# Kernel tuning notes

Hardware: AMD Instinct MI355X
Metric: run time of the kernel (lower is better)

The kernel has to match this reference:

```python
import jax, jax.numpy as jnp
import numpy as np

N, H, HEADS = 4096, 256, 3
ALPHA = 0.2
NEG_INF = -9e15


def _sign_adj(key, n, density):
    # sparse signed adjacency with +1 on the diagonal (values in {-1,0,1})
    k1, k2 = jax.random.split(key)
    mask = jax.random.uniform(k1, (n, n)) < density
    sign = jnp.where(jax.random.uniform(k2, (n, n)) < 0.5, -1.0, 1.0)
    adj = jnp.where(mask, sign, 0.0).astype(jnp.float32)
    idx = jnp.arange(n)
    return adj.at[idx, idx].set(1.0)


def setup_inputs() -> dict:
    key = jax.random.key(0)
    ks = jax.random.split(key, 16)
    std = 0.01
    gain = 1.414
    return {
        "h": jax.random.normal(ks[0], (N, H), jnp.float32),
        "node_adj": _sign_adj(ks[1], N, 0.005),
        "edge_adj": _sign_adj(ks[2], N, 0.005),
        "gat_W": jax.random.normal(ks[3], (HEADS, H, H), jnp.float32) * (gain / np.sqrt(H, dtype=np.float32)),
        "gat_a": jax.random.normal(ks[4], (HEADS, 2 * H, 1), jnp.float32) * 0.1,
        "edge_Wih": jax.random.normal(ks[5], (3 * H, H), jnp.float32) * std,
        "edge_Whh": jax.random.normal(ks[6], (3 * H, H), jnp.float32) * std,
        "edge_bih": jnp.zeros((3 * H,), jnp.float32),
        "edge_bhh": jnp.zeros((3 * H,), jnp.float32),
        "node_Wih": jax.random.normal(ks[7], (3 * H, H), jnp.float32) * std,
        "node_Whh": jax.random.normal(ks[8], (3 * H, H), jnp.float32) * std,
        "node_bih": jnp.zeros((3 * H,), jnp.float32),
        "node_bhh": jnp.zeros((3 * H,), jnp.float32),
    }


def _gru_cell(x, hstate, Wih, Whh, bih, bhh):
    # torch.nn.GRUCell math, gate order [r, z, n]
    gi = x @ Wih.T + bih
    gh = hstate @ Whh.T + bhh
    ir, iz, inn = jnp.split(gi, 3, axis=1)
    hr, hz, hn = jnp.split(gh, 3, axis=1)
    r = jax.nn.sigmoid(ir + hr)
    z = jax.nn.sigmoid(iz + hz)
    n = jnp.tanh(inn + r * hn)
    return (1.0 - z) * n + z * hstate


def _gat_head(h, node_adj, edge_adj, W, a):
    hW = h @ W  # [N,H]
    hp = (node_adj > 0).astype(hW.dtype) @ hW
    hm = (node_adj < 0).astype(hW.dtype) @ hW
    e_plus = jax.nn.leaky_relu(jnp.concatenate([hp, hm], axis=1) @ a, ALPHA)[:, 0]   # [N]
    e_minus = jax.nn.leaky_relu(jnp.concatenate([hm, hp], axis=1) @ a, ALPHA)[:, 0]  # [N]
    # attention[i, j] depends only on column j (original builds this via repeat)
    att = jnp.where(edge_adj > 0, e_plus[None, :], NEG_INF)
    att = jnp.where(edge_adj < 0, e_minus[None, :], att)
    att = jax.nn.softmax(att, axis=1)
    return (att * edge_adj) @ hW  # concat=False -> no elu


def reference(h, node_adj, edge_adj, gat_W, gat_a,
              edge_Wih, edge_Whh, edge_bih, edge_bhh,
              node_Wih, node_Whh, node_bih, node_bhh):
    dn = jnp.diag(node_adj)  # [N]
    de = jnp.diag(edge_adj)  # [N]
    idx = jnp.arange(node_adj.shape[0])
    node_adj_norm = node_adj.at[idx, idx].add(-dn)  # zero diagonal
    edge_adj_norm = edge_adj.at[idx, idx].add(-de)

    # msg_type == 'diff'
    node_support = node_adj_norm @ h
    edge_output = _gru_cell(node_support, h, edge_Wih, edge_Whh, edge_bih, edge_bhh)

    edge_support = _gat_head(h, node_adj_norm, edge_adj_norm, gat_W[0], gat_a[0])
    for i in range(1, HEADS):
        edge_support = edge_support + _gat_head(h, node_adj_norm, edge_adj_norm, gat_W[i], gat_a[i])
    edge_support = edge_support / HEADS

    node_output = _gru_cell(edge_support, h, node_Wih, node_Whh, node_bih, node_bhh)

    # sp.mm(I_edge, edge_output) + sp.mm(I_node, node_output)
    return de[:, None] * edge_output + dn[:, None] * node_output
```

## Files before the change

### kernel.cpp

```cpp
#include <hip/hip_runtime.h>
#include <hip/hip_bf16.h>
#include <math.h>

#define NN 4096
#define HH 256
#define G3 768
#define NHEADS 3
#define MAXE 128
#define ALPHA 0.2f

typedef __bf16 bf16;
typedef __attribute__((ext_vector_type(2))) __bf16 bf16x2;
typedef __attribute__((ext_vector_type(4))) __bf16 bf16x4;
typedef __attribute__((ext_vector_type(8))) __bf16 bf16x8;
typedef __attribute__((ext_vector_type(4))) float f32x4;

__device__ __forceinline__ void async_copy16(void* lds, const void* g) {
    __builtin_amdgcn_global_load_lds((const __attribute__((address_space(1))) void*)g,
                                     (__attribute__((address_space(3))) void*)lds, 16, 0, 0);
}

__device__ inline float lrelu(float x) { return x > 0.f ? x : ALPHA * x; }
__device__ inline float sigm(float x) { return 1.f / (1.f + __expf(-x)); }

__global__ __launch_bounds__(256) void prep_k(
    const float* __restrict__ h,
    const float* __restrict__ eWih, const float* __restrict__ eWhh,
    const float* __restrict__ nWih, const float* __restrict__ nWhh,
    const float* __restrict__ gat_W, const float* __restrict__ gat_a,
    bf16* __restrict__ hb,
    bf16* __restrict__ Weib, bf16* __restrict__ Wehb,
    bf16* __restrict__ Wnib, bf16* __restrict__ Wnhb,
    bf16* __restrict__ Wtb, float* __restrict__ c0, float* __restrict__ c1) {
    __shared__ float tile[32][33];
    __shared__ float a_s[512];
    int b = blockIdx.x, t = threadIdx.x;
    if (b < 1024) {
        int idx = b * 256 + t;
        float4 v = *(const float4*)(h + (size_t)idx * 4);
        bf16x4 o = {(bf16)v.x, (bf16)v.y, (bf16)v.z, (bf16)v.w};
        *(bf16x4*)(hb + (size_t)idx * 4) = o;
    } else if (b < 1792) {
        int w = (b - 1024) / 192;
        int idx = ((b - 1024) % 192) * 256 + t;
        const float* in = w == 0 ? eWih : (w == 1 ? eWhh : (w == 2 ? nWih : nWhh));
        bf16* outp = w == 0 ? Weib : (w == 1 ? Wehb : (w == 2 ? Wnib : Wnhb));
        float4 v = *(const float4*)(in + (size_t)idx * 4);
        bf16x4 o = {(bf16)v.x, (bf16)v.y, (bf16)v.z, (bf16)v.w};
        *(bf16x4*)(outp + (size_t)idx * 4) = o;
    } else if (b < 1984) {
        int b2 = b - 1792;
        int hd = b2 >> 6, tl = b2 & 63;
        int k0 = (tl >> 3) * 32, n0 = (tl & 7) * 32;
        int tx = t % 32, ty = t / 32;
        const float* Wh = gat_W + (size_t)hd * HH * HH;
        for (int r = ty; r < 32; r += 8) tile[r][tx] = Wh[(size_t)(k0 + r) * HH + n0 + tx];
        __syncthreads();
        bf16* Wth = Wtb + (size_t)hd * HH * HH;
        for (int r = ty; r < 32; r += 8) Wth[(size_t)(n0 + r) * HH + k0 + tx] = (bf16)tile[tx][r];
    } else {
        int hd = b - 1984;
        a_s[t] = gat_a[(size_t)hd * 512 + t];
        a_s[t + 256] = gat_a[(size_t)hd * 512 + 256 + t];
        __syncthreads();
        const float* Wr = gat_W + (size_t)hd * HH * HH + (size_t)t * HH;
        f32x4 s0v = {}, s1v = {};
#pragma unroll 8
        for (int c4 = 0; c4 < 64; c4++) {
            f32x4 w = *(const f32x4*)(Wr + c4 * 4);
            f32x4 a0 = *(const f32x4*)(a_s + c4 * 4);
            f32x4 a1 = *(const f32x4*)(a_s + 256 + c4 * 4);
            s0v += w * a0;
            s1v += w * a1;
        }
        c0[hd * HH + t] = s0v[0] + s0v[1] + s0v[2] + s0v[3];
        c1[hd * HH + t] = s1v[0] + s1v[1] + s1v[2] + s1v[3];
    }
}

__global__ __launch_bounds__(256) void compact_k(
    const float* __restrict__ node_adj, const float* __restrict__ edge_adj,
    float* __restrict__ dn, float* __restrict__ de,
    int* __restrict__ ccols_n, int* __restrict__ nnz_n,
    int* __restrict__ ccols_e, int* __restrict__ nnz_e) {
    int b = blockIdx.x, t = threadIdx.x;
    bool node = b < NN;
    int i = node ? b : b - NN;
    __shared__ int cnt;
    __shared__ int cols_s[MAXE];
    if (t == 0) cnt = 0;
    __syncthreads();
    const float* rp = (node ? node_adj : edge_adj) + (size_t)i * NN + t * 16;

    f32x4 v0 = *(const f32x4*)(rp);
    f32x4 v1 = *(const f32x4*)(rp + 4);
    f32x4 v2 = *(const f32x4*)(rp + 8);
    f32x4 v3 = *(const f32x4*)(rp + 12);
    int j0 = t * 16;

    int k = 0;
#define CNT(A, J) { float a_ = (A); if (a_ != 0.f) { if ((J) == i) (node ? dn : de)[i] = a_; else k++; } }
    CNT(v0[0], j0)      CNT(v0[1], j0 + 1)  CNT(v0[2], j0 + 2)  CNT(v0[3], j0 + 3)
    CNT(v1[0], j0 + 4)  CNT(v1[1], j0 + 5)  CNT(v1[2], j0 + 6)  CNT(v1[3], j0 + 7)
    CNT(v2[0], j0 + 8)  CNT(v2[1], j0 + 9)  CNT(v2[2], j0 + 10) CNT(v2[3], j0 + 11)
    CNT(v3[0], j0 + 12) CNT(v3[1], j0 + 13) CNT(v3[2], j0 + 14) CNT(v3[3], j0 + 15)
#undef CNT

    int base = 0;
    if (k) base = atomicAdd(&cnt, k);

#define WRT(A, J) { float a_ = (A); if (a_ != 0.f && (J) != i) { \
        if (base < MAXE) cols_s[base] = (a_ > 0.f) ? ((J) + 1) : -((J) + 1); base++; } }
    WRT(v0[0], j0)      WRT(v0[1], j0 + 1)  WRT(v0[2], j0 + 2)  WRT(v0[3], j0 + 3)
    WRT(v1[0], j0 + 4)  WRT(v1[1], j0 + 5)  WRT(v1[2], j0 + 6)  WRT(v1[3], j0 + 7)
    WRT(v2[0], j0 + 8)  WRT(v2[1], j0 + 9)  WRT(v2[2], j0 + 10) WRT(v2[3], j0 + 11)
    WRT(v3[0], j0 + 12) WRT(v3[1], j0 + 13) WRT(v3[2], j0 + 14) WRT(v3[3], j0 + 15)
#undef WRT

    __syncthreads();
    int n = cnt < MAXE ? cnt : MAXE;
    int* cg = (node ? ccols_n : ccols_e) + (size_t)i * MAXE;
    if (t == 0) (node ? nnz_n : nnz_e)[i] = n;
    if (t < n) cg[t] = cols_s[t];
}

__global__ __launch_bounds__(256) void gather_k(
    const int* __restrict__ ccols_n, const int* __restrict__ nnz_n,
    const bf16* __restrict__ hb,
    const float* __restrict__ c0, const float* __restrict__ c1,
    bf16* __restrict__ nsupb, float* __restrict__ ep, float* __restrict__ em) {
    int i = blockIdx.x, t = threadIdx.x, lane = t & 63, wid = t >> 6;
    __shared__ int cols_s[MAXE];
    __shared__ float part[6][4];
    int n = nnz_n[i];
    if (n > MAXE) n = MAXE;
    if (t < n) cols_s[t] = ccols_n[(size_t)i * MAXE + t];
    __syncthreads();
    float accp = 0.f, accm = 0.f;
#pragma unroll 8
    for (int kk = 0; kk < n; kk++) {
        int c = cols_s[kk];
        int j = (c > 0 ? c : -c) - 1;
        float hv = (float)hb[(size_t)j * HH + t];
        if (c > 0) accp += hv; else accm += hv;
    }
    nsupb[(size_t)i * HH + t] = (bf16)(accp - accm);
    float u[6];
#pragma unroll
    for (int hd = 0; hd < NHEADS; hd++) {
        float a0 = c0[hd * HH + t], a1 = c1[hd * HH + t];
        u[hd * 2]     = accp * a0 + accm * a1;
        u[hd * 2 + 1] = accm * a0 + accp * a1;
    }
#pragma unroll
    for (int vv = 0; vv < 6; vv++)
#pragma unroll
        for (int off = 32; off; off >>= 1) u[vv] += __shfl_xor(u[vv], off);
    if (lane == 0)
#pragma unroll
        for (int vv = 0; vv < 6; vv++) part[vv][wid] = u[vv];
    __syncthreads();
    if (t < 6) {
        float s = part[t][0] + part[t][1] + part[t][2] + part[t][3];
        int hd = t >> 1;
        ((t & 1) == 0 ? ep : em)[(size_t)hd * NN + i] = lrelu(s);
    }
}

__global__ __launch_bounds__(256) void gemm_bt(
    const bf16* __restrict__ A0, const bf16* __restrict__ A1, const bf16* __restrict__ A2,
    const bf16* __restrict__ B0, const bf16* __restrict__ B1, const bf16* __restrict__ B2,
    bf16* __restrict__ C0, bf16* __restrict__ C1, bf16* __restrict__ C2) {
    __shared__ bf16 a_s[128 * 32];
    __shared__ bf16 b_s[128 * 32];
    int z = blockIdx.z;
    const bf16* A = z == 0 ? A0 : (z == 1 ? A1 : A2);
    const bf16* Bt = z == 0 ? B0 : (z == 1 ? B1 : B2);
    bf16* C = z == 0 ? C0 : (z == 1 ? C1 : C2);

    int tid = threadIdx.x;
    int lane = tid & 63, wid = tid >> 6;
    int wr = (wid >> 1) * 64, wc = (wid & 1) * 64;
    int i0 = blockIdx.x * 128;
    int c0n = blockIdx.y * 128;

    f32x4 acc[4][4] = {};
    int kq = (lane >> 4) * 8;

    for (int k0 = 0; k0 < 256; k0 += 32) {
        __syncthreads();
#pragma unroll
        for (int it = 0; it < 2; it++) {
            int ch = it * 256 + tid;
            int r = ch >> 2, c16 = ch & 3;
            async_copy16(&a_s[ch * 8], A + (size_t)(i0 + r) * 256 + k0 + c16 * 8);
            async_copy16(&b_s[ch * 8], Bt + (size_t)(c0n + r) * 256 + k0 + c16 * 8);
        }
        __syncthreads();
        bf16x8 af[4], bf[4];
#pragma unroll
        for (int m = 0; m < 4; m++) af[m] = *(const bf16x8*)&a_s[(wr + m * 16 + (lane & 15)) * 32 + kq];
#pragma unroll
        for (int n = 0; n < 4; n++) bf[n] = *(const bf16x8*)&b_s[(wc + n * 16 + (lane & 15)) * 32 + kq];
#pragma unroll
        for (int m = 0; m < 4; m++)
#pragma unroll
            for (int n = 0; n < 4; n++)
                acc[m][n] = __builtin_amdgcn_mfma_f32_16x16x32_bf16(af[m], bf[n], acc[m][n], 0, 0, 0);
    }
#pragma unroll
    for (int m = 0; m < 4; m++) {
#pragma unroll
        for (int n = 0; n < 4; n++) {
            int row = i0 + wr + m * 16 + (lane >> 4) * 4;
            int col = c0n + wc + n * 16 + (lane & 15);
#pragma unroll
            for (int j = 0; j < 4; j++)
                C[(size_t)(row + j) * G3 + col] = (bf16)acc[m][n][j];
        }
    }
}

__global__ __launch_bounds__(256) void gat_out(
    const int* __restrict__ ccols_e, const int* __restrict__ nnz_e,
    const float* __restrict__ ep, const float* __restrict__ em,
    const bf16* __restrict__ hWb2, bf16* __restrict__ esupb) {
    int i = blockIdx.x, t = threadIdx.x;
    __shared__ int cols_s[MAXE];
    __shared__ int js[MAXE];
    __shared__ float w_s[NHEADS][MAXE];
    __shared__ f32x4 sacc[NHEADS][64];
    int n = nnz_e[i];
    if (n > MAXE) n = MAXE;
    if (t < n) {
        int c = ccols_e[(size_t)i * MAXE + t];
        cols_s[t] = c;
        js[t] = (c > 0 ? c : -c) - 1;
    }
    __syncthreads();
    int wid = t >> 6, lane = t & 63;
    if (wid < NHEADS) {
        int hd = wid;
        const float* eph = ep + (size_t)hd * NN;
        const float* emh = em + (size_t)hd * NN;
        float v0 = -1e30f, v1 = -1e30f;
        if (lane < n)      { int c = cols_s[lane];      v0 = c > 0 ? eph[js[lane]]      : emh[js[lane]]; }
        if (lane + 64 < n) { int c = cols_s[lane + 64]; v1 = c > 0 ? eph[js[lane + 64]] : emh[js[lane + 64]]; }
        float mx = fmaxf(v0, v1);
#pragma unroll
        for (int off = 32; off; off >>= 1) mx = fmaxf(mx, __shfl_xor(mx, off));
        float w0 = (lane < n) ? __expf(v0 - mx) : 0.f;
        float w1 = (lane + 64 < n) ? __expf(v1 - mx) : 0.f;
        float s = w0 + w1;
#pragma unroll
        for (int off = 32; off; off >>= 1) s += __shfl_xor(s, off);
        float inv = 1.f / s;
        if (lane < n)      w_s[hd][lane]      = (cols_s[lane] > 0 ? w0 : -w0) * inv;
        if (lane + 64 < n) w_s[hd][lane + 64] = (cols_s[lane + 64] > 0 ? w1 : -w1) * inv;
    }
    __syncthreads();
    if (t < 192) {
        int hd = t >> 6, g = t & 63;
        const bf16* base = hWb2 + (size_t)hd * HH + g * 4;
        f32x4 acc = {};
#pragma unroll 4
        for (int k = 0; k < n; k++) {
            float w = w_s[hd][k];
            bf16x4 hv = *(const bf16x4*)(base + (size_t)js[k] * G3);
            f32x4 f = {(float)hv[0], (float)hv[1], (float)hv[2], (float)hv[3]};
            acc += w * f;
        }
        sacc[hd][g] = acc;
    }
    __syncthreads();
    if (t < 64) {
        f32x4 s = (sacc[0][t] + sacc[1][t] + sacc[2][t]) * (1.f / 3.f);
        bf16x4 o = {(bf16)s[0], (bf16)s[1], (bf16)s[2], (bf16)s[3]};
        *(bf16x4*)(esupb + (size_t)i * HH + t * 4) = o;
    }
}

__global__ __launch_bounds__(256) void gru_both(
    const bf16* __restrict__ gie, const bf16* __restrict__ ghe,
    const bf16* __restrict__ gin, const bf16* __restrict__ ghn,
    const float* __restrict__ ebih, const float* __restrict__ ebhh,
    const float* __restrict__ nbih, const float* __restrict__ nbhh,
    const float* __restrict__ h, const float* __restrict__ dnv, const float* __restrict__ dev,
    float* __restrict__ out) {
    int sub = threadIdx.x >> 7, tc = threadIdx.x & 127;
    int i = blockIdx.x * 2 + sub;
    int c = tc * 2;
    size_t gb = (size_t)i * G3;
    float2 hv = *(const float2*)(h + (size_t)i * HH + c);
    float De = dev[i], Dn = dnv[i];

#define LD2(p, off) (*(const bf16x2*)((p) + gb + (off) + c))
#define BI2(p, off) (*(const float2*)((p) + (off) + c))
    bf16x2 eir = LD2(gie, 0), eiz = LD2(gie, 256), ein = LD2(gie, 512);
    bf16x2 ehr = LD2(ghe, 0), ehz = LD2(ghe, 256), ehn = LD2(ghe, 512);
    bf16x2 nir = LD2(gin, 0), niz = LD2(gin, 256), nin = LD2(gin, 512);
    bf16x2 nhr = LD2(ghn, 0), nhz = LD2(ghn, 256), nhn = LD2(ghn, 512);
    float2 ebr = BI2(ebih, 0), ebz = BI2(ebih, 256), ebn = BI2(ebih, 512);
    float2 eb2r = BI2(ebhh, 0), eb2z = BI2(ebhh, 256), eb2n = BI2(ebhh, 512);
    float2 nbr = BI2(nbih, 0), nbz = BI2(nbih, 256), nbn = BI2(nbih, 512);
    float2 nb2r = BI2(nbhh, 0), nb2z = BI2(nbhh, 256), nb2n = BI2(nbhh, 512);
#undef LD2
#undef BI2

    float res[2];
#pragma unroll
    for (int j = 0; j < 2; j++) {
        float hj = j == 0 ? hv.x : hv.y;
        float r = sigm(((float)eir[j] + (j ? ebr.y : ebr.x)) + ((float)ehr[j] + (j ? eb2r.y : eb2r.x)));
        float z = sigm(((float)eiz[j] + (j ? ebz.y : ebz.x)) + ((float)ehz[j] + (j ? eb2z.y : eb2z.x)));
        float nv = tanhf(((float)ein[j] + (j ? ebn.y : ebn.x)) + r * ((float)ehn[j] + (j ? eb2n.y : eb2n.x)));
        float eo = (1.f - z) * nv + z * hj;
        float r2 = sigm(((float)nir[j] + (j ? nbr.y : nbr.x)) + ((float)nhr[j] + (j ? nb2r.y : nb2r.x)));
        float z2 = sigm(((float)niz[j] + (j ? nbz.y : nbz.x)) + ((float)nhz[j] + (j ? nb2z.y : nb2z.x)));
        float nv2 = tanhf(((float)nin[j] + (j ? nbn.y : nbn.x)) + r2 * ((float)nhn[j] + (j ? nb2n.y : nb2n.x)));
        float no = (1.f - z2) * nv2 + z2 * hj;
        res[j] = De * eo + Dn * no;
    }
    *(float2*)(out + (size_t)i * HH + c) = make_float2(res[0], res[1]);
}

extern "C" void kernel_launch(void* const* d_in, const int* in_sizes, int n_in,
                              void* d_out, int out_size, void* d_ws, size_t ws_size,
                              hipStream_t stream) {
    const float* h        = (const float*)d_in[0];
    const float* node_adj = (const float*)d_in[1];
    const float* edge_adj = (const float*)d_in[2];
    const float* gat_W    = (const float*)d_in[3];
    const float* gat_a    = (const float*)d_in[4];
    const float* e_Wih    = (const float*)d_in[5];
    const float* e_Whh    = (const float*)d_in[6];
    const float* e_bih    = (const float*)d_in[7];
    const float* e_bhh    = (const float*)d_in[8];
    const float* n_Wih    = (const float*)d_in[9];
    const float* n_Whh    = (const float*)d_in[10];
    const float* n_bih    = (const float*)d_in[11];
    const float* n_bhh    = (const float*)d_in[12];
    float* out = (float*)d_out;

    char* ws = (char*)d_ws;
    size_t off = 0;
    auto alloc = [&](size_t bytes) { char* p = ws + off; off += (bytes + 255) & ~(size_t)255; return p; };

    float* ep    = (float*)alloc((size_t)NHEADS * NN * 4);
    float* em    = (float*)alloc((size_t)NHEADS * NN * 4);
    float* c0    = (float*)alloc((size_t)NHEADS * HH * 4);
    float* c1    = (float*)alloc((size_t)NHEADS * HH * 4);
    float* dn    = (float*)alloc(NN * 4);
    float* de    = (float*)alloc(NN * 4);
    bf16*  hb    = (bf16*)alloc((size_t)NN * HH * 2);
    bf16*  nsupb = (bf16*)alloc((size_t)NN * HH * 2);
    bf16*  esupb = (bf16*)alloc((size_t)NN * HH * 2);
    bf16*  hWb2  = (bf16*)alloc((size_t)NN * G3 * 2);
    bf16*  gie   = (bf16*)alloc((size_t)NN * G3 * 2);
    bf16*  ghe   = (bf16*)alloc((size_t)NN * G3 * 2);
    bf16*  gin   = (bf16*)alloc((size_t)NN * G3 * 2);
    bf16*  ghn   = (bf16*)alloc((size_t)NN * G3 * 2);
    bf16*  Weib  = (bf16*)alloc((size_t)G3 * HH * 2);
    bf16*  Wehb  = (bf16*)alloc((size_t)G3 * HH * 2);
    bf16*  Wnib  = (bf16*)alloc((size_t)G3 * HH * 2);
    bf16*  Wnhb  = (bf16*)alloc((size_t)G3 * HH * 2);
    bf16*  Wtb   = (bf16*)alloc((size_t)NHEADS * HH * HH * 2);
    int*   ccols_n = (int*)alloc((size_t)NN * MAXE * 4);
    int*   nnz_n   = (int*)alloc(NN * 4);
    int*   ccols_e = (int*)alloc((size_t)NN * MAXE * 4);
    int*   nnz_e   = (int*)alloc(NN * 4);

    dim3 b256(256);

    compact_k<<<2 * NN, b256, 0, stream>>>(node_adj, edge_adj, dn, de,
                                           ccols_n, nnz_n, ccols_e, nnz_e);

    prep_k<<<1987, b256, 0, stream>>>(h, e_Wih, e_Whh, n_Wih, n_Whh, gat_W, gat_a,
                                      hb, Weib, Wehb, Wnib, Wnhb, Wtb, c0, c1);

    gather_k<<<NN, b256, 0, stream>>>(ccols_n, nnz_n, hb, c0, c1, nsupb, ep, em);

    gemm_bt<<<dim3(NN / 128, G3 / 128, 3), b256, 0, stream>>>(
        hb, nsupb, hb, Wtb, Weib, Wehb, hWb2, gie, ghe);

    gat_out<<<NN, b256, 0, stream>>>(ccols_e, nnz_e, ep, em, hWb2, esupb);

    gemm_bt<<<dim3(NN / 128, G3 / 128, 2), b256, 0, stream>>>(
        esupb, hb, hb, Wnib, Wnhb, Wnhb, gin, ghn, ghn);

    gru_both<<<NN / 2, b256, 0, stream>>>(gie, ghe, gin, ghn,
                                          e_bih, e_bhh, n_bih, n_bhh,
                                          h, dn, de, out);
}
```

Before: 95.43 us.

## Fuse adjacency compaction with h-dependent GEMMs into one heterogeneous kernel

Merges the adjacency compaction kernel with the three GEMMs that depend only on h (hW for the GAT heads, and the hidden-state projections for both GRUs) into one launch. Blocks are split by index into GEMM tiles and compaction rows. The remaining GEMM launch now handles only the two input-dependent projections (node support and edge support). This removes launches and lets the memory-bound compaction overlap with MFMA work, but the compaction rows are permuted and the GEMM tiles use a simpler non-pipelined loop.

```diff
diff --git a/kernel.cpp b/kernel.cpp
--- a/kernel.cpp
+++ b/kernel.cpp
@@ -78,50 +78,102 @@
     }
 }
 
-__global__ __launch_bounds__(256) void compact_k(
+#define NGEMM 576
+__global__ __launch_bounds__(256) void mega_k(
     const float* __restrict__ node_adj, const float* __restrict__ edge_adj,
     float* __restrict__ dn, float* __restrict__ de,
     int* __restrict__ ccols_n, int* __restrict__ nnz_n,
-    int* __restrict__ ccols_e, int* __restrict__ nnz_e) {
-    int b = blockIdx.x, t = threadIdx.x;
-    bool node = b < NN;
-    int i = node ? b : b - NN;
+    int* __restrict__ ccols_e, int* __restrict__ nnz_e,
+    const bf16* __restrict__ hb, const bf16* __restrict__ Wtb,
+    const bf16* __restrict__ Wehb, const bf16* __restrict__ Wnhb,
+    bf16* __restrict__ hWb2, bf16* __restrict__ ghe, bf16* __restrict__ ghn) {
+    __shared__ bf16 a_s[128 * 32];
+    __shared__ bf16 b_s[128 * 32];
     __shared__ int cnt;
     __shared__ int cols_s[MAXE];
-    if (t == 0) cnt = 0;
-    __syncthreads();
-    const float* rp = (node ? node_adj : edge_adj) + (size_t)i * NN + t * 16;
-
-    f32x4 v0 = *(const f32x4*)(rp);
-    f32x4 v1 = *(const f32x4*)(rp + 4);
-    f32x4 v2 = *(const f32x4*)(rp + 8);
-    f32x4 v3 = *(const f32x4*)(rp + 12);
-    int j0 = t * 16;
-
-    int k = 0;
+    int bid = blockIdx.x, t = threadIdx.x;
+
+    if (bid < NGEMM) {
+        int z = bid / 192, r = bid % 192;
+        int i0 = (r % 32) * 128;
+        int c0n = (r / 32) * 128;
+        const bf16* Bt = z == 0 ? Wtb : (z == 1 ? Wehb : Wnhb);
+        bf16* C = z == 0 ? hWb2 : (z == 1 ? ghe : ghn);
+
+        int lane = t & 63, wid = t >> 6;
+        int wr = (wid >> 1) * 64, wc = (wid & 1) * 64;
+        f32x4 acc[4][4] = {};
+        int kq = (lane >> 4) * 8;
+
+        for (int k0 = 0; k0 < 256; k0 += 32) {
+            __syncthreads();
+#pragma unroll
+            for (int it = 0; it < 2; it++) {
+                int ch = it * 256 + t;
+                int rr = ch >> 2, c16 = ch & 3;
+                async_copy16(&a_s[ch * 8], hb + (size_t)(i0 + rr) * 256 + k0 + c16 * 8);
+                async_copy16(&b_s[ch * 8], Bt + (size_t)(c0n + rr) * 256 + k0 + c16 * 8);
+            }
+            __syncthreads();
+            bf16x8 af[4], bf[4];
+#pragma unroll
+            for (int m = 0; m < 4; m++) af[m] = *(const bf16x8*)&a_s[(wr + m * 16 + (lane & 15)) * 32 + kq];
+#pragma unroll
+            for (int n = 0; n < 4; n++) bf[n] = *(const bf16x8*)&b_s[(wc + n * 16 + (lane & 15)) * 32 + kq];
+#pragma unroll
+            for (int m = 0; m < 4; m++)
+#pragma unroll
+                for (int n = 0; n < 4; n++)
+                    acc[m][n] = __builtin_amdgcn_mfma_f32_16x16x32_bf16(af[m], bf[n], acc[m][n], 0, 0, 0);
+        }
+#pragma unroll
+        for (int m = 0; m < 4; m++) {
+#pragma unroll
+            for (int n = 0; n < 4; n++) {
+                int row = i0 + wr + m * 16 + (lane >> 4) * 4;
+                int col = c0n + wc + n * 16 + (lane & 15);
+#pragma unroll
+                for (int j = 0; j < 4; j++)
+                    C[(size_t)(row + j) * G3 + col] = (bf16)acc[m][n][j];
+            }
+        }
+    } else {
+        int g2 = bid - NGEMM;
+        int gs = (g2 & 7) * 1024 + (g2 >> 3);
+        bool node = gs < NN;
+        int i = node ? gs : gs - NN;
+        if (t == 0) cnt = 0;
+        __syncthreads();
+        const float* rp = (node ? node_adj : edge_adj) + (size_t)i * NN + t * 16;
+
+        f32x4 v0 = *(const f32x4*)(rp);
+        f32x4 v1 = *(const f32x4*)(rp + 4);
+        f32x4 v2 = *(const f32x4*)(rp + 8);
+        f32x4 v3 = *(const f32x4*)(rp + 12);
+        int j0 = t * 16;
+
+        int k = 0;
 #define CNT(A, J) { float a_ = (A); if (a_ != 0.f) { if ((J) == i) (node ? dn : de)[i] = a_; else k++; } }
-    CNT(v0[0], j0)      CNT(v0[1], j0 + 1)  CNT(v0[2], j0 + 2)  CNT(v0[3], j0 + 3)
-    CNT(v1[0], j0 + 4)  CNT(v1[1], j0 + 5)  CNT(v1[2], j0 + 6)  CNT(v1[3], j0 + 7)
-    CNT(v2[0], j0 + 8)  CNT(v2[1], j0 + 9)  CNT(v2[2], j0 + 10) CNT(v2[3], j0 + 11)
-    CNT(v3[0], j0 + 12) CNT(v3[1], j0 + 13) CNT(v3[2], j0 + 14) CNT(v3[3], j0 + 15)
+        CNT(v0[0], j0)      CNT(v0[1], j0 + 1)  CNT(v0[2], j0 + 2)  CNT(v0[3], j0 + 3)
+        CNT(v1[0], j0 + 4)  CNT(v1[1], j0 + 5)  CNT(v1[2], j0 + 6)  CNT(v1[3], j0 + 7)
+        CNT(v2[0], j0 + 8)  CNT(v2[1], j0 + 9)  CNT(v2[2], j0 + 10) CNT(v2[3], j0 + 11)
+        CNT(v3[0], j0 + 12) CNT(v3[1], j0 + 13) CNT(v3[2], j0 + 14) CNT(v3[3], j0 + 15)
 #undef CNT
-
-    int base = 0;
-    if (k) base = atomicAdd(&cnt, k);
-
+        int base = 0;
+        if (k) base = atomicAdd(&cnt, k);
 #define WRT(A, J) { float a_ = (A); if (a_ != 0.f && (J) != i) { \
-        if (base < MAXE) cols_s[base] = (a_ > 0.f) ? ((J) + 1) : -((J) + 1); base++; } }
-    WRT(v0[0], j0)      WRT(v0[1], j0 + 1)  WRT(v0[2], j0 + 2)  WRT(v0[3], j0 + 3)
-    WRT(v1[0], j0 + 4)  WRT(v1[1], j0 + 5)  WRT(v1[2], j0 + 6)  WRT(v1[3], j0 + 7)
-    WRT(v2[0], j0 + 8)  WRT(v2[1], j0 + 9)  WRT(v2[2], j0 + 10) WRT(v2[3], j0 + 11)
-    WRT(v3[0], j0 + 12) WRT(v3[1], j0 + 13) WRT(v3[2], j0 + 14) WRT(v3[3], j0 + 15)
+            if (base < MAXE) cols_s[base] = (a_ > 0.f) ? ((J) + 1) : -((J) + 1); base++; } }
+        WRT(v0[0], j0)      WRT(v0[1], j0 + 1)  WRT(v0[2], j0 + 2)  WRT(v0[3], j0 + 3)
+        WRT(v1[0], j0 + 4)  WRT(v1[1], j0 + 5)  WRT(v1[2], j0 + 6)  WRT(v1[3], j0 + 7)
+        WRT(v2[0], j0 + 8)  WRT(v2[1], j0 + 9)  WRT(v2[2], j0 + 10) WRT(v2[3], j0 + 11)
+        WRT(v3[0], j0 + 12) WRT(v3[1], j0 + 13) WRT(v3[2], j0 + 14) WRT(v3[3], j0 + 15)
 #undef WRT
-
-    __syncthreads();
-    int n = cnt < MAXE ? cnt : MAXE;
-    int* cg = (node ? ccols_n : ccols_e) + (size_t)i * MAXE;
-    if (t == 0) (node ? nnz_n : nnz_e)[i] = n;
-    if (t < n) cg[t] = cols_s[t];
+        __syncthreads();
+        int n = cnt < MAXE ? cnt : MAXE;
+        int* cg = (node ? ccols_n : ccols_e) + (size_t)i * MAXE;
+        if (t == 0) (node ? nnz_n : nnz_e)[i] = n;
+        if (t < n) cg[t] = cols_s[t];
+    }
 }
 
 __global__ __launch_bounds__(256) void gather_k(
@@ -372,21 +424,19 @@
 
     dim3 b256(256);
 
-    compact_k<<<2 * NN, b256, 0, stream>>>(node_adj, edge_adj, dn, de,
-                                           ccols_n, nnz_n, ccols_e, nnz_e);
-
     prep_k<<<1987, b256, 0, stream>>>(h, e_Wih, e_Whh, n_Wih, n_Whh, gat_W, gat_a,
                                       hb, Weib, Wehb, Wnib, Wnhb, Wtb, c0, c1);
 
+    mega_k<<<NGEMM + 2 * NN, b256, 0, stream>>>(node_adj, edge_adj, dn, de,
+                                                ccols_n, nnz_n, ccols_e, nnz_e,
+                                                hb, Wtb, Wehb, Wnhb, hWb2, ghe, ghn);
+
     gather_k<<<NN, b256, 0, stream>>>(ccols_n, nnz_n, hb, c0, c1, nsupb, ep, em);
 
-    gemm_bt<<<dim3(NN / 128, G3 / 128, 3), b256, 0, stream>>>(
-        hb, nsupb, hb, Wtb, Weib, Wehb, hWb2, gie, ghe);
-
     gat_out<<<NN, b256, 0, stream>>>(ccols_e, nnz_e, ep, em, hWb2, esupb);
 
     gemm_bt<<<dim3(NN / 128, G3 / 128, 2), b256, 0, stream>>>(
-        esupb, hb, hb, Wnib, Wnhb, Wnhb, gin, ghn, ghn);
+        nsupb, esupb, esupb, Weib, Wnib, Wnib, gie, gin, gin);
 
     gru_both<<<NN / 2, b256, 0, stream>>>(gie, ghe, gin, ghn,
                                           e_bih, e_bhh, n_bih, n_bhh,
```

New measurement: 92.87 us. 1.03x faster.

## Fuse adjacency compaction with node gather into one wave-per-row scan kernel

Applied to the files above, without the earlier changes.

Merges the row compaction kernel and the node-support gather kernel into a single scan kernel. Each wave handles four adjacency rows, double-buffering row loads in registers, and consumes the node column list straight from LDS, so the node column list is never written to global memory. The GEMM inputs are regrouped so the first GEMM uses only h (hW, hidden-gate products for both GRUs) and the second takes nsup and esup. This removes a launch and a global round trip, but uses fewer, larger blocks (512 blocks, launch bounds of 1 block per CU) with heavy register use, which may lower occupancy.

```diff
diff --git a/kernel.cpp b/kernel.cpp
--- a/kernel.cpp
+++ b/kernel.cpp
@@ -78,93 +78,113 @@
     }
 }
 
-__global__ __launch_bounds__(256) void compact_k(
+__global__ __launch_bounds__(256, 1) void scan_k(
     const float* __restrict__ node_adj, const float* __restrict__ edge_adj,
-    float* __restrict__ dn, float* __restrict__ de,
-    int* __restrict__ ccols_n, int* __restrict__ nnz_n,
-    int* __restrict__ ccols_e, int* __restrict__ nnz_e) {
-    int b = blockIdx.x, t = threadIdx.x;
-    bool node = b < NN;
-    int i = node ? b : b - NN;
-    __shared__ int cnt;
-    __shared__ int cols_s[MAXE];
-    if (t == 0) cnt = 0;
-    __syncthreads();
-    const float* rp = (node ? node_adj : edge_adj) + (size_t)i * NN + t * 16;
-
-    f32x4 v0 = *(const f32x4*)(rp);
-    f32x4 v1 = *(const f32x4*)(rp + 4);
-    f32x4 v2 = *(const f32x4*)(rp + 8);
-    f32x4 v3 = *(const f32x4*)(rp + 12);
-    int j0 = t * 16;
-
-    int k = 0;
-#define CNT(A, J) { float a_ = (A); if (a_ != 0.f) { if ((J) == i) (node ? dn : de)[i] = a_; else k++; } }
-    CNT(v0[0], j0)      CNT(v0[1], j0 + 1)  CNT(v0[2], j0 + 2)  CNT(v0[3], j0 + 3)
-    CNT(v1[0], j0 + 4)  CNT(v1[1], j0 + 5)  CNT(v1[2], j0 + 6)  CNT(v1[3], j0 + 7)
-    CNT(v2[0], j0 + 8)  CNT(v2[1], j0 + 9)  CNT(v2[2], j0 + 10) CNT(v2[3], j0 + 11)
-    CNT(v3[0], j0 + 12) CNT(v3[1], j0 + 13) CNT(v3[2], j0 + 14) CNT(v3[3], j0 + 15)
-#undef CNT
-
-    int base = 0;
-    if (k) base = atomicAdd(&cnt, k);
-
-#define WRT(A, J) { float a_ = (A); if (a_ != 0.f && (J) != i) { \
-        if (base < MAXE) cols_s[base] = (a_ > 0.f) ? ((J) + 1) : -((J) + 1); base++; } }
-    WRT(v0[0], j0)      WRT(v0[1], j0 + 1)  WRT(v0[2], j0 + 2)  WRT(v0[3], j0 + 3)
-    WRT(v1[0], j0 + 4)  WRT(v1[1], j0 + 5)  WRT(v1[2], j0 + 6)  WRT(v1[3], j0 + 7)
-    WRT(v2[0], j0 + 8)  WRT(v2[1], j0 + 9)  WRT(v2[2], j0 + 10) WRT(v2[3], j0 + 11)
-    WRT(v3[0], j0 + 12) WRT(v3[1], j0 + 13) WRT(v3[2], j0 + 14) WRT(v3[3], j0 + 15)
-#undef WRT
-
-    __syncthreads();
-    int n = cnt < MAXE ? cnt : MAXE;
-    int* cg = (node ? ccols_n : ccols_e) + (size_t)i * MAXE;
-    if (t == 0) (node ? nnz_n : nnz_e)[i] = n;
-    if (t < n) cg[t] = cols_s[t];
-}
-
-__global__ __launch_bounds__(256) void gather_k(
-    const int* __restrict__ ccols_n, const int* __restrict__ nnz_n,
     const bf16* __restrict__ hb,
     const float* __restrict__ c0, const float* __restrict__ c1,
-    bf16* __restrict__ nsupb, float* __restrict__ ep, float* __restrict__ em) {
-    int i = blockIdx.x, t = threadIdx.x, lane = t & 63, wid = t >> 6;
-    __shared__ int cols_s[MAXE];
-    __shared__ float part[6][4];
-    int n = nnz_n[i];
-    if (n > MAXE) n = MAXE;
-    if (t < n) cols_s[t] = ccols_n[(size_t)i * MAXE + t];
-    __syncthreads();
-    float accp = 0.f, accm = 0.f;
-#pragma unroll 8
-    for (int kk = 0; kk < n; kk++) {
-        int c = cols_s[kk];
-        int j = (c > 0 ? c : -c) - 1;
-        float hv = (float)hb[(size_t)j * HH + t];
-        if (c > 0) accp += hv; else accm += hv;
-    }
-    nsupb[(size_t)i * HH + t] = (bf16)(accp - accm);
-    float u[6];
-#pragma unroll
-    for (int hd = 0; hd < NHEADS; hd++) {
-        float a0 = c0[hd * HH + t], a1 = c1[hd * HH + t];
-        u[hd * 2]     = accp * a0 + accm * a1;
-        u[hd * 2 + 1] = accm * a0 + accp * a1;
-    }
-#pragma unroll
-    for (int vv = 0; vv < 6; vv++)
-#pragma unroll
-        for (int off = 32; off; off >>= 1) u[vv] += __shfl_xor(u[vv], off);
-    if (lane == 0)
-#pragma unroll
-        for (int vv = 0; vv < 6; vv++) part[vv][wid] = u[vv];
-    __syncthreads();
-    if (t < 6) {
-        float s = part[t][0] + part[t][1] + part[t][2] + part[t][3];
-        int hd = t >> 1;
-        ((t & 1) == 0 ? ep : em)[(size_t)hd * NN + i] = lrelu(s);
-    }
+    bf16* __restrict__ nsupb, float* __restrict__ dn, float* __restrict__ de,
+    float* __restrict__ ep, float* __restrict__ em,
+    int* __restrict__ ccols_e, int* __restrict__ nnz_e) {
+    __shared__ int cnt[4];
+    __shared__ int cols[4][MAXE];
+    int t = threadIdx.x, lane = t & 63, wid = t >> 6;
+    int gid = blockIdx.x * 4 + wid;
+    bool isnode = gid < 1024;
+    int ibase = (isnode ? gid : gid - 1024) * 4;
+    const float* adj = isnode ? node_adj : edge_adj;
+    float* diag = isnode ? dn : de;
+    int* cntw = &cnt[wid];
+    int* colw = cols[wid];
+
+    f32x4 ca0 = {}, ca1 = {}, ca2 = {}, cb0 = {}, cb1 = {}, cb2 = {};
+    if (isnode) {
+        ca0 = *(const f32x4*)(c0 + 0 * HH + lane * 4);
+        ca1 = *(const f32x4*)(c0 + 1 * HH + lane * 4);
+        ca2 = *(const f32x4*)(c0 + 2 * HH + lane * 4);
+        cb0 = *(const f32x4*)(c1 + 0 * HH + lane * 4);
+        cb1 = *(const f32x4*)(c1 + 1 * HH + lane * 4);
+        cb2 = *(const f32x4*)(c1 + 2 * HH + lane * 4);
+    }
+
+    f32x4 A0, A1, A2, A3, A4, A5, A6, A7, A8, A9, A10, A11, A12, A13, A14, A15;
+    f32x4 B0, B1, B2, B3, B4, B5, B6, B7, B8, B9, B10, B11, B12, B13, B14, B15;
+
+#define ROWLD(P_, R_) { const float* rp_ = adj + (size_t)(ibase + (R_)) * NN + lane * 4; \
+    P_##0 = *(const f32x4*)(rp_);        P_##1 = *(const f32x4*)(rp_ + 256); \
+    P_##2 = *(const f32x4*)(rp_ + 512);  P_##3 = *(const f32x4*)(rp_ + 768); \
+    P_##4 = *(const f32x4*)(rp_ + 1024); P_##5 = *(const f32x4*)(rp_ + 1280); \
+    P_##6 = *(const f32x4*)(rp_ + 1536); P_##7 = *(const f32x4*)(rp_ + 1792); \
+    P_##8 = *(const f32x4*)(rp_ + 2048); P_##9 = *(const f32x4*)(rp_ + 2304); \
+    P_##10 = *(const f32x4*)(rp_ + 2560); P_##11 = *(const f32x4*)(rp_ + 2816); \
+    P_##12 = *(const f32x4*)(rp_ + 3072); P_##13 = *(const f32x4*)(rp_ + 3328); \
+    P_##14 = *(const f32x4*)(rp_ + 3584); P_##15 = *(const f32x4*)(rp_ + 3840); }
+
+#define PEL1(A_, J_) { float a_ = (A_); if (a_ != 0.f) { if ((J_) == i) diag[i] = a_; else kc++; } }
+#define PEL2(A_, J_) { float a_ = (A_); if (a_ != 0.f && (J_) != i) { \
+    if (base < MAXE) colw[base] = (a_ > 0.f) ? ((J_) + 1) : -((J_) + 1); base++; } }
+#define PQ1(P_, Q_) { int jb_ = (Q_) * 256 + lane * 4; \
+    PEL1(P_##Q_[0], jb_) PEL1(P_##Q_[1], jb_ + 1) PEL1(P_##Q_[2], jb_ + 2) PEL1(P_##Q_[3], jb_ + 3) }
+#define PQ2(P_, Q_) { int jb_ = (Q_) * 256 + lane * 4; \
+    PEL2(P_##Q_[0], jb_) PEL2(P_##Q_[1], jb_ + 1) PEL2(P_##Q_[2], jb_ + 2) PEL2(P_##Q_[3], jb_ + 3) }
+
+#define PROC(P_, R_) { \
+    int i = ibase + (R_); \
+    if (lane == 0) *cntw = 0; \
+    int kc = 0; \
+    PQ1(P_,0) PQ1(P_,1) PQ1(P_,2) PQ1(P_,3) PQ1(P_,4) PQ1(P_,5) PQ1(P_,6) PQ1(P_,7) \
+    PQ1(P_,8) PQ1(P_,9) PQ1(P_,10) PQ1(P_,11) PQ1(P_,12) PQ1(P_,13) PQ1(P_,14) PQ1(P_,15) \
+    int base = 0; \
+    if (kc) base = atomicAdd(cntw, kc); \
+    PQ2(P_,0) PQ2(P_,1) PQ2(P_,2) PQ2(P_,3) PQ2(P_,4) PQ2(P_,5) PQ2(P_,6) PQ2(P_,7) \
+    PQ2(P_,8) PQ2(P_,9) PQ2(P_,10) PQ2(P_,11) PQ2(P_,12) PQ2(P_,13) PQ2(P_,14) PQ2(P_,15) \
+    int n = *cntw; \
+    if (n > MAXE) n = MAXE; \
+    if (isnode) { \
+        f32x4 accp = {}, accm = {}; \
+        for (int kk = 0; kk < n; kk++) { \
+            int c_ = colw[kk]; \
+            int j_ = (c_ > 0 ? c_ : -c_) - 1; \
+            bf16x4 hv_ = *(const bf16x4*)(hb + (size_t)j_ * HH + lane * 4); \
+            f32x4 f_ = {(float)hv_[0], (float)hv_[1], (float)hv_[2], (float)hv_[3]}; \
+            if (c_ > 0) accp += f_; else accm += f_; \
+        } \
+        f32x4 d_ = accp - accm; \
+        bf16x4 o_ = {(bf16)d_[0], (bf16)d_[1], (bf16)d_[2], (bf16)d_[3]}; \
+        *(bf16x4*)(nsupb + (size_t)i * HH + lane * 4) = o_; \
+        f32x4 u0v = accp * ca0 + accm * cb0, u1v = accm * ca0 + accp * cb0; \
+        f32x4 u2v = accp * ca1 + accm * cb1, u3v = accm * ca1 + accp * cb1; \
+        f32x4 u4v = accp * ca2 + accm * cb2, u5v = accm * ca2 + accp * cb2; \
+        float u[6]; \
+        u[0] = u0v[0] + u0v[1] + u0v[2] + u0v[3]; u[1] = u1v[0] + u1v[1] + u1v[2] + u1v[3]; \
+        u[2] = u2v[0] + u2v[1] + u2v[2] + u2v[3]; u[3] = u3v[0] + u3v[1] + u3v[2] + u3v[3]; \
+        u[4] = u4v[0] + u4v[1] + u4v[2] + u4v[3]; u[5] = u5v[0] + u5v[1] + u5v[2] + u5v[3]; \
+        _Pragma("unroll") \
+        for (int vv = 0; vv < 6; vv++) \
+            _Pragma("unroll") \
+            for (int off_ = 32; off_; off_ >>= 1) u[vv] += __shfl_xor(u[vv], off_); \
+        if (lane == 0) { \
+            ep[0 * NN + i] = lrelu(u[0]); em[0 * NN + i] = lrelu(u[1]); \
+            ep[1 * NN + i] = lrelu(u[2]); em[1 * NN + i] = lrelu(u[3]); \
+            ep[2 * NN + i] = lrelu(u[4]); em[2 * NN + i] = lrelu(u[5]); \
+        } \
+    } else { \
+        if (lane == 0) nnz_e[i] = n; \
+        for (int kk = lane; kk < n; kk += 64) ccols_e[(size_t)i * MAXE + kk] = colw[kk]; \
+    } \
+}
+
+    ROWLD(A, 0)
+    ROWLD(B, 1) PROC(A, 0)
+    ROWLD(A, 2) PROC(B, 1)
+    ROWLD(B, 3) PROC(A, 2)
+    PROC(B, 3)
+
+#undef PROC
+#undef PQ2
+#undef PQ1
+#undef PEL2
+#undef PEL1
+#undef ROWLD
 }
 
 __global__ __launch_bounds__(256) void gemm_bt(
@@ -365,28 +385,24 @@
     bf16*  Wnib  = (bf16*)alloc((size_t)G3 * HH * 2);
     bf16*  Wnhb  = (bf16*)alloc((size_t)G3 * HH * 2);
     bf16*  Wtb   = (bf16*)alloc((size_t)NHEADS * HH * HH * 2);
-    int*   ccols_n = (int*)alloc((size_t)NN * MAXE * 4);
-    int*   nnz_n   = (int*)alloc(NN * 4);
     int*   ccols_e = (int*)alloc((size_t)NN * MAXE * 4);
     int*   nnz_e   = (int*)alloc(NN * 4);
 
     dim3 b256(256);
 
-    compact_k<<<2 * NN, b256, 0, stream>>>(node_adj, edge_adj, dn, de,
-                                           ccols_n, nnz_n, ccols_e, nnz_e);
-
     prep_k<<<1987, b256, 0, stream>>>(h, e_Wih, e_Whh, n_Wih, n_Whh, gat_W, gat_a,
                                       hb, Weib, Wehb, Wnib, Wnhb, Wtb, c0, c1);
 
-    gather_k<<<NN, b256, 0, stream>>>(ccols_n, nnz_n, hb, c0, c1, nsupb, ep, em);
+    scan_k<<<512, b256, 0, stream>>>(node_adj, edge_adj, hb, c0, c1,
+                                     nsupb, dn, de, ep, em, ccols_e, nnz_e);
 
     gemm_bt<<<dim3(NN / 128, G3 / 128, 3), b256, 0, stream>>>(
-        hb, nsupb, hb, Wtb, Weib, Wehb, hWb2, gie, ghe);
+        hb, hb, hb, Wtb, Wehb, Wnhb, hWb2, ghe, ghn);
 
     gat_out<<<NN, b256, 0, stream>>>(ccols_e, nnz_e, ep, em, hWb2, esupb);
 
     gemm_bt<<<dim3(NN / 128, G3 / 128, 2), b256, 0, stream>>>(
-        esupb, hb, hb, Wnib, Wnhb, Wnhb, gin, ghn, ghn);
+        nsupb, esupb, esupb, Weib, Wnib, Wnib, gie, gin, gin);
 
     gru_both<<<NN / 2, b256, 0, stream>>>(gie, ghe, gin, ghn,
                                           e_bih, e_bhh, n_bih, n_bhh,
```

After: 100.1 us. 1.05x slower.

## Compact adjacency rows with global atomics and regroup GEMMs by dependency

Applied to the files above, without the earlier changes.

The compaction kernel now has each block handle two rows of both adjacencies and append column indices straight to global memory through global atomics on per-row counters. This removes the shared-memory staging and block syncs and cuts the block count to a quarter. The counters are zeroed by extra blocks in the prep kernel, which now runs first. The GEMMs are regrouped so that all products that depend only on h (hW, the two hidden-state GEMMs) run in one launch before the gather. The input-side GEMMs for nsup and esup are batched into a single launch after gat_out. Column order within a row now depends on atomic timing, which may change summation order, and the global atomics add contention.

```diff
diff --git a/kernel.cpp b/kernel.cpp
--- a/kernel.cpp
+++ b/kernel.cpp
@@ -31,7 +31,8 @@
     bf16* __restrict__ hb,
     bf16* __restrict__ Weib, bf16* __restrict__ Wehb,
     bf16* __restrict__ Wnib, bf16* __restrict__ Wnhb,
-    bf16* __restrict__ Wtb, float* __restrict__ c0, float* __restrict__ c1) {
+    bf16* __restrict__ Wtb, float* __restrict__ c0, float* __restrict__ c1,
+    int* __restrict__ nnz_n, int* __restrict__ nnz_e) {
     __shared__ float tile[32][33];
     __shared__ float a_s[512];
     int b = blockIdx.x, t = threadIdx.x;
@@ -58,7 +59,7 @@
         __syncthreads();
         bf16* Wth = Wtb + (size_t)hd * HH * HH;
         for (int r = ty; r < 32; r += 8) Wth[(size_t)(n0 + r) * HH + k0 + tx] = (bf16)tile[tx][r];
-    } else {
+    } else if (b < 1987) {
         int hd = b - 1984;
         a_s[t] = gat_a[(size_t)hd * 512 + t];
         a_s[t + 256] = gat_a[(size_t)hd * 512 + 256 + t];
@@ -75,6 +76,42 @@
         }
         c0[hd * HH + t] = s0v[0] + s0v[1] + s0v[2] + s0v[3];
         c1[hd * HH + t] = s1v[0] + s1v[1] + s1v[2] + s1v[3];
+    } else {
+        int b2 = b - 1987;
+        int* dst = (b2 < 4) ? nnz_n : nnz_e;
+        int idx = (b2 & 3) * 256 + t;
+        ((int4*)dst)[idx] = make_int4(0, 0, 0, 0);
+    }
+}
+
+__device__ __forceinline__ void proc_chunk(f32x4 w0, f32x4 w1, f32x4 w2, f32x4 w3,
+                                           int row, int col0,
+                                           float* __restrict__ diagp,
+                                           int* __restrict__ nnzp,
+                                           int* __restrict__ colsp) {
+    int kc = 0;
+#define E1(V) { float a_ = (V); int col_ = col0 + ec_; ec_++; if (a_ != 0.f) { \
+        if (col_ == row) diagp[row] = a_; else kc++; } }
+    {
+        int ec_ = 0;
+        E1(w0[0]) E1(w0[1]) E1(w0[2]) E1(w0[3])
+        E1(w1[0]) E1(w1[1]) E1(w1[2]) E1(w1[3])
+        E1(w2[0]) E1(w2[1]) E1(w2[2]) E1(w2[3])
+        E1(w3[0]) E1(w3[1]) E1(w3[2]) E1(w3[3])
+    }
+#undef E1
+    if (kc) {
+        int base = atomicAdd(nnzp + row, kc);
+#define E2(V) { float a_ = (V); int col_ = col0 + ec_; ec_++; if (a_ != 0.f && col_ != row) { \
+        if (base < MAXE) colsp[(size_t)row * MAXE + base] = (a_ > 0.f) ? (col_ + 1) : -(col_ + 1); base++; } }
+        {
+            int ec_ = 0;
+            E2(w0[0]) E2(w0[1]) E2(w0[2]) E2(w0[3])
+            E2(w1[0]) E2(w1[1]) E2(w1[2]) E2(w1[3])
+            E2(w2[0]) E2(w2[1]) E2(w2[2]) E2(w2[3])
+            E2(w3[0]) E2(w3[1]) E2(w3[2]) E2(w3[3])
+        }
+#undef E2
     }
 }
 
@@ -84,44 +121,26 @@
     int* __restrict__ ccols_n, int* __restrict__ nnz_n,
     int* __restrict__ ccols_e, int* __restrict__ nnz_e) {
     int b = blockIdx.x, t = threadIdx.x;
-    bool node = b < NN;
-    int i = node ? b : b - NN;
-    __shared__ int cnt;
-    __shared__ int cols_s[MAXE];
-    if (t == 0) cnt = 0;
-    __syncthreads();
-    const float* rp = (node ? node_adj : edge_adj) + (size_t)i * NN + t * 16;
-
-    f32x4 v0 = *(const f32x4*)(rp);
-    f32x4 v1 = *(const f32x4*)(rp + 4);
-    f32x4 v2 = *(const f32x4*)(rp + 8);
-    f32x4 v3 = *(const f32x4*)(rp + 12);
-    int j0 = t * 16;
-
-    int k = 0;
-#define CNT(A, J) { float a_ = (A); if (a_ != 0.f) { if ((J) == i) (node ? dn : de)[i] = a_; else k++; } }
-    CNT(v0[0], j0)      CNT(v0[1], j0 + 1)  CNT(v0[2], j0 + 2)  CNT(v0[3], j0 + 3)
-    CNT(v1[0], j0 + 4)  CNT(v1[1], j0 + 5)  CNT(v1[2], j0 + 6)  CNT(v1[3], j0 + 7)
-    CNT(v2[0], j0 + 8)  CNT(v2[1], j0 + 9)  CNT(v2[2], j0 + 10) CNT(v2[3], j0 + 11)
-    CNT(v3[0], j0 + 12) CNT(v3[1], j0 + 13) CNT(v3[2], j0 + 14) CNT(v3[3], j0 + 15)
-#undef CNT
-
-    int base = 0;
-    if (k) base = atomicAdd(&cnt, k);
-
-#define WRT(A, J) { float a_ = (A); if (a_ != 0.f && (J) != i) { \
-        if (base < MAXE) cols_s[base] = (a_ > 0.f) ? ((J) + 1) : -((J) + 1); base++; } }
-    WRT(v0[0], j0)      WRT(v0[1], j0 + 1)  WRT(v0[2], j0 + 2)  WRT(v0[3], j0 + 3)
-    WRT(v1[0], j0 + 4)  WRT(v1[1], j0 + 5)  WRT(v1[2], j0 + 6)  WRT(v1[3], j0 + 7)
-    WRT(v2[0], j0 + 8)  WRT(v2[1], j0 + 9)  WRT(v2[2], j0 + 10) WRT(v2[3], j0 + 11)
-    WRT(v3[0], j0 + 12) WRT(v3[1], j0 + 13) WRT(v3[2], j0 + 14) WRT(v3[3], j0 + 15)
-#undef WRT
-
-    __syncthreads();
-    int n = cnt < MAXE ? cnt : MAXE;
-    int* cg = (node ? ccols_n : ccols_e) + (size_t)i * MAXE;
-    if (t == 0) (node ? nnz_n : nnz_e)[i] = n;
-    if (t < n) cg[t] = cols_s[t];
+    int col0 = t * 16;
+    int r0 = b, r1 = b + 2048;
+
+    const float* s0 = node_adj + ((size_t)r0 << 12) + col0;
+    const float* s1 = node_adj + ((size_t)r1 << 12) + col0;
+    const float* s2 = edge_adj + ((size_t)r0 << 12) + col0;
+    const float* s3 = edge_adj + ((size_t)r1 << 12) + col0;
+
+    f32x4 A0, A1, A2, A3, B0, B1, B2, B3;
+#define LD(P_, SRC_) { P_##0 = *(const f32x4*)(SRC_); P_##1 = *(const f32x4*)((SRC_) + 4); \
+                       P_##2 = *(const f32x4*)((SRC_) + 8); P_##3 = *(const f32x4*)((SRC_) + 12); }
+    LD(A, s0)
+    LD(B, s1)
+    proc_chunk(A0, A1, A2, A3, r0, col0, dn, nnz_n, ccols_n);
+    LD(A, s2)
+    proc_chunk(B0, B1, B2, B3, r1, col0, dn, nnz_n, ccols_n);
+    LD(B, s3)
+    proc_chunk(A0, A1, A2, A3, r0, col0, de, nnz_e, ccols_e);
+    proc_chunk(B0, B1, B2, B3, r1, col0, de, nnz_e, ccols_e);
+#undef LD
 }
 
 __global__ __launch_bounds__(256) void gather_k(
@@ -372,21 +391,22 @@
 
     dim3 b256(256);
 
-    compact_k<<<2 * NN, b256, 0, stream>>>(node_adj, edge_adj, dn, de,
-                                           ccols_n, nnz_n, ccols_e, nnz_e);
-
-    prep_k<<<1987, b256, 0, stream>>>(h, e_Wih, e_Whh, n_Wih, n_Whh, gat_W, gat_a,
-                                      hb, Weib, Wehb, Wnib, Wnhb, Wtb, c0, c1);
+    prep_k<<<1995, b256, 0, stream>>>(h, e_Wih, e_Whh, n_Wih, n_Whh, gat_W, gat_a,
+                                      hb, Weib, Wehb, Wnib, Wnhb, Wtb, c0, c1,
+                                      nnz_n, nnz_e);
+
+    compact_k<<<2048, b256, 0, stream>>>(node_adj, edge_adj, dn, de,
+                                         ccols_n, nnz_n, ccols_e, nnz_e);
+
+    gemm_bt<<<dim3(NN / 128, G3 / 128, 3), b256, 0, stream>>>(
+        hb, hb, hb, Wtb, Wehb, Wnhb, hWb2, ghe, ghn);
 
     gather_k<<<NN, b256, 0, stream>>>(ccols_n, nnz_n, hb, c0, c1, nsupb, ep, em);
 
-    gemm_bt<<<dim3(NN / 128, G3 / 128, 3), b256, 0, stream>>>(
-        hb, nsupb, hb, Wtb, Weib, Wehb, hWb2, gie, ghe);
-
     gat_out<<<NN, b256, 0, stream>>>(ccols_e, nnz_e, ep, em, hWb2, esupb);
 
     gemm_bt<<<dim3(NN / 128, G3 / 128, 2), b256, 0, stream>>>(
-        esupb, hb, hb, Wnib, Wnhb, Wnhb, gin, ghn, ghn);
+        nsupb, esupb, esupb, Weib, Wnib, Wnib, gie, gin, gin);
 
     gru_both<<<NN / 2, b256, 0, stream>>>(gie, ghe, gin, ghn,
                                           e_bih, e_bhh, n_bih, n_bhh,
```

After: 100.7 us. 5.5% more time.
